# Performance work log

Measured on AMD Instinct MI355X. Metric: run time of the kernel, lower is better.

The kernel has to match this reference:

```python
import jax, jax.numpy as jnp
import numpy as np

EMBED = 1024
HEADS = 16
HEAD_DIM = EMBED // HEADS


def setup_inputs() -> dict:
    key = jax.random.key(0)
    ks = jax.random.split(key, 11)
    B, S = 2, 2048
    scale = 1.0 / np.sqrt(EMBED)
    inp = {
        'Q': jax.random.normal(ks[0], (B, S, EMBED), jnp.float32),
        'K': jax.random.normal(ks[1], (B, S, EMBED), jnp.float32),
        'V': jax.random.normal(ks[2], (B, S, EMBED), jnp.float32),
        'Wq': jax.random.normal(ks[3], (EMBED, EMBED), jnp.float32) * scale,
        'bq': jnp.zeros((EMBED,), jnp.float32),
        'Wk': jax.random.normal(ks[4], (EMBED, EMBED), jnp.float32) * scale,
        'bk': jnp.zeros((EMBED,), jnp.float32),
        'Wv': jax.random.normal(ks[5], (EMBED, EMBED), jnp.float32) * scale,
        'bv': jnp.zeros((EMBED,), jnp.float32),
        'Wo': jax.random.normal(ks[6], (EMBED, EMBED), jnp.float32) * scale,
        'bo': jnp.zeros((EMBED,), jnp.float32),
    }
    return inp


def reference(Q, K, V, Wq, bq, Wk, bk, Wv, bv, Wo, bo):
    B, Sq, _ = Q.shape
    Sk = K.shape[1]
    # linear projections (torch nn.Linear: x @ W.T + b; here W stored as [in,out])
    q = Q @ Wq + bq
    k = K @ Wk + bk
    v = V @ Wv + bv
    # [B, H, S, D]
    q = q.reshape(B, Sq, HEADS, HEAD_DIM).transpose(0, 2, 1, 3)
    k = k.reshape(B, Sk, HEADS, HEAD_DIM).transpose(0, 2, 1, 3)
    v = v.reshape(B, Sk, HEADS, HEAD_DIM).transpose(0, 2, 1, 3)
    scores = jnp.einsum('bhqd,bhkd->bhqk', q, k) / jnp.sqrt(jnp.float32(HEAD_DIM))
    attn = jax.nn.softmax(scores, axis=-1)
    out = jnp.einsum('bhqk,bhkd->bhqd', attn, v)
    out = out.transpose(0, 2, 1, 3).reshape(B, Sq, EMBED)
    return out @ Wo + bo
```

## Files before the change

### kernel.cpp

```cpp
#include <hip/hip_runtime.h>

#define EMBED 1024
#define HEADS 16
#define HDIM  64
#define BATCH 2
#define SEQ   2048
#define MTOK  (BATCH*SEQ)

typedef _Float16 half_t;
typedef __attribute__((ext_vector_type(4))) float    f32x4;
typedef __attribute__((ext_vector_type(8))) _Float16 f16x8;
typedef __attribute__((ext_vector_type(4))) _Float16 f16x4;

#define MFMA16(a,b,c) __builtin_amdgcn_mfma_f32_16x16x32_f16(a,b,c,0,0,0)

#define GLOAD_LDS16(gp, lp)                                                     \
    __builtin_amdgcn_global_load_lds(                                           \
        (const __attribute__((address_space(1))) void*)(gp),                    \
        (__attribute__((address_space(3))) void*)(lp), 16, 0, 0)

#define QSCALE 0.18033688f

__global__ __launch_bounds__(256) void wt_kernel(const float* __restrict__ W0,
                                                 const float* __restrict__ W1,
                                                 const float* __restrict__ W2,
                                                 const float* __restrict__ W3,
                                                 half_t* __restrict__ T0,
                                                 half_t* __restrict__ T1,
                                                 half_t* __restrict__ T2,
                                                 half_t* __restrict__ T3)
{
    const int z = blockIdx.z;
    const float* W = (z == 0) ? W0 : (z == 1) ? W1 : (z == 2) ? W2 : W3;
    half_t* WT     = (z == 0) ? T0 : (z == 1) ? T1 : (z == 2) ? T2 : T3;

    __shared__ float tile[64][68];
    const int t  = threadIdx.x;
    const int n0 = blockIdx.x * 64;
    const int k0 = blockIdx.y * 64;
#pragma unroll
    for (int i = 0; i < 4; ++i) {
        int f = t + 256 * i;
        int r = f >> 4, c4 = (f & 15) << 2;
        float4 v = *(const float4*)(W + (size_t)(k0 + r) * EMBED + n0 + c4);
        tile[r][c4 + 0] = v.x; tile[r][c4 + 1] = v.y;
        tile[r][c4 + 2] = v.z; tile[r][c4 + 3] = v.w;
    }
    __syncthreads();
#pragma unroll
    for (int i = 0; i < 4; ++i) {
        int f = t + 256 * i;
        int nr = f >> 4, kc = (f & 15) << 2;
        f16x4 o;
        o[0] = (half_t)tile[kc + 0][nr];
        o[1] = (half_t)tile[kc + 1][nr];
        o[2] = (half_t)tile[kc + 2][nr];
        o[3] = (half_t)tile[kc + 3][nr];
        *(f16x4*)(WT + (size_t)(n0 + nr) * EMBED + k0 + kc) = o;
    }
}

__global__ __launch_bounds__(256) void conv_kernel(const float* __restrict__ S0,
                                                   const float* __restrict__ S1,
                                                   const float* __restrict__ S2,
                                                   half_t* __restrict__ D0,
                                                   half_t* __restrict__ D1,
                                                   half_t* __restrict__ D2)
{
    const int z = blockIdx.z;
    const float* S = (z == 0) ? S0 : (z == 1) ? S1 : S2;
    half_t* D      = (z == 0) ? D0 : (z == 1) ? D1 : D2;
    size_t idx = ((size_t)blockIdx.x * 256 + threadIdx.x) * 8;
    float4 v0 = *(const float4*)(S + idx);
    float4 v1 = *(const float4*)(S + idx + 4);
    f16x8 hv;
    hv[0] = (half_t)v0.x; hv[1] = (half_t)v0.y;
    hv[2] = (half_t)v0.z; hv[3] = (half_t)v0.w;
    hv[4] = (half_t)v1.x; hv[5] = (half_t)v1.y;
    hv[6] = (half_t)v1.z; hv[7] = (half_t)v1.w;
    *(f16x8*)(D + idx) = hv;
}

__global__ __launch_bounds__(256, 3) void proj3_kernel(const half_t* __restrict__ Aq,
                                                       const half_t* __restrict__ Ak,
                                                       const half_t* __restrict__ Av,
                                                       const half_t* __restrict__ Btq,
                                                       const half_t* __restrict__ Btk,
                                                       const half_t* __restrict__ Btv,
                                                       const float*  __restrict__ bq,
                                                       const float*  __restrict__ bk,
                                                       const float*  __restrict__ bv,
                                                       half_t* __restrict__ oq,
                                                       half_t* __restrict__ ok,
                                                       half_t* __restrict__ ov)
{
    const int z = blockIdx.z;
    const half_t* A    = (z == 0) ? Aq  : (z == 1) ? Ak  : Av;
    const half_t* Bt   = (z == 0) ? Btq : (z == 1) ? Btk : Btv;
    const float*  bias = (z == 0) ? bq  : (z == 1) ? bk  : bv;
    half_t*       out  = (z == 0) ? oq  : (z == 1) ? ok  : ov;

    __shared__ half_t As[128 * 64];
    __shared__ half_t Bs[128 * 64];
    const int tid = threadIdx.x, lane = tid & 63, g = lane >> 4, ln = lane & 15;
    const int w = tid >> 6, wm = w >> 1, wn = w & 1;
    const int n0 = blockIdx.x * 128, m0 = blockIdx.y * 128;
    const int srow8 = lane >> 3, schunk = lane & 7;

    f32x4 acc[4][4];
#pragma unroll
    for (int i = 0; i < 4; ++i)
#pragma unroll
        for (int j = 0; j < 4; ++j) acc[i][j] = (f32x4){0.f, 0.f, 0.f, 0.f};

    for (int kt = 0; kt < EMBED; kt += 64) {
#pragma unroll
        for (int i = 0; i < 4; ++i) {
            int row = (i * 4 + w) * 8 + srow8;
            GLOAD_LDS16(A  + (size_t)(m0 + row) * EMBED + kt + schunk * 8,
                        (char*)As + (i * 4 + w) * 1024);
            GLOAD_LDS16(Bt + (size_t)(n0 + row) * EMBED + kt + schunk * 8,
                        (char*)Bs + (i * 4 + w) * 1024);
        }
        __syncthreads();
#pragma unroll
        for (int k2 = 0; k2 < 2; ++k2) {
            f16x8 af[4], bf[4];
#pragma unroll
            for (int mi = 0; mi < 4; ++mi)
                af[mi] = *(const f16x8*)(As + (wm * 64 + mi * 16 + ln) * 64 + k2 * 32 + g * 8);
#pragma unroll
            for (int ni = 0; ni < 4; ++ni)
                bf[ni] = *(const f16x8*)(Bs + (wn * 64 + ni * 16 + ln) * 64 + k2 * 32 + g * 8);
#pragma unroll
            for (int mi = 0; mi < 4; ++mi)
#pragma unroll
                for (int ni = 0; ni < 4; ++ni)
                    acc[mi][ni] = MFMA16(af[mi], bf[ni], acc[mi][ni]);
        }
        __syncthreads();
    }

#pragma unroll
    for (int mi = 0; mi < 4; ++mi) {
#pragma unroll
        for (int ni = 0; ni < 4; ++ni) {
            int col = n0 + wn * 64 + ni * 16 + ln;
            float bb = bias[col];
            int h = col >> 6, d = col & 63;
#pragma unroll
            for (int r = 0; r < 4; ++r) {
                int row = m0 + wm * 64 + mi * 16 + g * 4 + r;
                int b = row >> 11, s = row & 2047;
                float val = acc[mi][ni][r] + bb;
                if (z == 0) val *= QSCALE;
                if (z == 2)
                    out[((size_t)(b * HEADS + h) * HDIM + d) * SEQ + s] = (half_t)val;
                else
                    out[((size_t)(b * HEADS + h) * SEQ + s) * HDIM + d] = (half_t)val;
            }
        }
    }
}

__global__ __launch_bounds__(256, 4) void final_kernel(const half_t* __restrict__ A,
                                                       const half_t* __restrict__ Bt,
                                                       const float*  __restrict__ bias,
                                                       float* __restrict__ out)
{
    __shared__ half_t As[64 * 64];
    __shared__ half_t Bs[128 * 64];
    const int tid = threadIdx.x, lane = tid & 63, g = lane >> 4, ln = lane & 15;
    const int w = tid >> 6, wm = w >> 1, wn = w & 1;
    const int n0 = blockIdx.x * 128, m0 = blockIdx.y * 64;
    const int srow8 = lane >> 3, schunk = lane & 7;

    f32x4 acc[2][4];
#pragma unroll
    for (int i = 0; i < 2; ++i)
#pragma unroll
        for (int j = 0; j < 4; ++j) acc[i][j] = (f32x4){0.f, 0.f, 0.f, 0.f};

    for (int kt = 0; kt < EMBED; kt += 64) {
#pragma unroll
        for (int i = 0; i < 2; ++i) {
            int rg = i * 4 + w;
            GLOAD_LDS16(A + (size_t)(m0 + rg * 8 + srow8) * EMBED + kt + schunk * 8,
                        (char*)As + rg * 1024);
        }
#pragma unroll
        for (int i = 0; i < 4; ++i) {
            int rg = i * 4 + w;
            GLOAD_LDS16(Bt + (size_t)(n0 + rg * 8 + srow8) * EMBED + kt + schunk * 8,
                        (char*)Bs + rg * 1024);
        }
        __syncthreads();
#pragma unroll
        for (int k2 = 0; k2 < 2; ++k2) {
            f16x8 af[2], bf[4];
#pragma unroll
            for (int mi = 0; mi < 2; ++mi)
                af[mi] = *(const f16x8*)(As + (wm * 32 + mi * 16 + ln) * 64 + k2 * 32 + g * 8);
#pragma unroll
            for (int ni = 0; ni < 4; ++ni)
                bf[ni] = *(const f16x8*)(Bs + (wn * 64 + ni * 16 + ln) * 64 + k2 * 32 + g * 8);
#pragma unroll
            for (int mi = 0; mi < 2; ++mi)
#pragma unroll
                for (int ni = 0; ni < 4; ++ni)
                    acc[mi][ni] = MFMA16(af[mi], bf[ni], acc[mi][ni]);
        }
        __syncthreads();
    }
#pragma unroll
    for (int mi = 0; mi < 2; ++mi) {
#pragma unroll
        for (int ni = 0; ni < 4; ++ni) {
            int col = n0 + wn * 64 + ni * 16 + ln;
            float bb = bias[col];
#pragma unroll
            for (int r = 0; r < 4; ++r) {
                int row = m0 + wm * 32 + mi * 16 + g * 4 + r;
                out[(size_t)row * EMBED + col] = acc[mi][ni][r] + bb;
            }
        }
    }
}

__global__ __launch_bounds__(256, 2) void attn_kernel(const half_t* __restrict__ q,
                                                      const half_t* __restrict__ k,
                                                      const half_t* __restrict__ vt,
                                                      half_t* __restrict__ opart,
                                                      float*  __restrict__ lpart)
{
    __shared__ half_t Ks[64 * 64];
    __shared__ half_t Vs[64 * 64];
    __shared__ half_t Ps[4][32 * 72];
    const int tid = threadIdx.x, lane = tid & 63, g = lane >> 4, ln = lane & 15;
    const int w = tid >> 6;

    const int fid = blockIdx.x;
    const int j = fid & 7, t = fid >> 3;
    const int yhi = t >> 5, rem = t & 31;
    const int z = rem >> 4, x = rem & 15;
    const int bh = yhi * 8 + j;
    const int bb = bh >> 4, h = bh & 15;

    const int kv0 = z * (SEQ / 2);
    const int kvend = kv0 + SEQ / 2;
    const half_t* qh = q  + (size_t)bh * SEQ * HDIM;
    const half_t* kh = k  + (size_t)bh * SEQ * HDIM;
    const half_t* vh = vt + (size_t)bh * HDIM * SEQ;
    const int qrow0 = x * 128 + w * 32;

    f16x8 qfrag[2][2];
#pragma unroll
    for (int mt = 0; mt < 2; ++mt)
#pragma unroll
        for (int kt = 0; kt < 2; ++kt)
            qfrag[mt][kt] = *(const f16x8*)(qh + (size_t)(qrow0 + mt * 16 + ln) * HDIM + kt * 32 + g * 8);

    f32x4 accO[2][4];
#pragma unroll
    for (int mt = 0; mt < 2; ++mt)
#pragma unroll
        for (int nt = 0; nt < 4; ++nt) accO[mt][nt] = (f32x4){0.f, 0.f, 0.f, 0.f};
    float lsum[2] = {0.f, 0.f};

    const int srow0 = tid >> 3;
    const int scol16 = tid & 7;

    {
        f16x8 rK[2], rV[2];
#pragma unroll
        for (int c = 0; c < 2; ++c) {
            int row = c * 32 + srow0;
            rK[c] = *(const f16x8*)(kh + (size_t)(kv0 + row) * HDIM + scol16 * 8);
            rV[c] = *(const f16x8*)(vh + (size_t)row * SEQ + kv0 + scol16 * 8);
        }
#pragma unroll
        for (int c = 0; c < 2; ++c) {
            int row = c * 32 + srow0;
            int off = row * 128 + ((scol16 * 16) ^ ((row & 7) << 4));
            *(f16x8*)((char*)Ks + off) = rK[c];
            *(f16x8*)((char*)Vs + off) = rV[c];
        }
    }
    __syncthreads();

    for (int kv = kv0; kv < kvend; kv += 64) {
        f32x4 accT[2][4];
#pragma unroll
        for (int mt = 0; mt < 2; ++mt)
#pragma unroll
            for (int kb = 0; kb < 4; ++kb) accT[mt][kb] = (f32x4){0.f, 0.f, 0.f, 0.f};
#pragma unroll
        for (int kt = 0; kt < 2; ++kt) {
            f16x8 kf[4];
#pragma unroll
            for (int kb = 0; kb < 4; ++kb) {
                int row = kb * 16 + ln;
                kf[kb] = *(const f16x8*)((char*)Ks + row * 128 + ((kt * 64 + g * 16) ^ ((row & 7) << 4)));
            }
            __builtin_amdgcn_s_setprio(1);
#pragma unroll
            for (int mt = 0; mt < 2; ++mt)
#pragma unroll
                for (int kb = 0; kb < 4; ++kb)
                    accT[mt][kb] = MFMA16(kf[kb], qfrag[mt][kt], accT[mt][kb]);
            __builtin_amdgcn_s_setprio(0);
        }

        const bool has_next = (kv + 64) < kvend;
        f16x8 rK[2], rV[2];
        if (has_next) {
#pragma unroll
            for (int c = 0; c < 2; ++c) {
                int row = c * 32 + srow0;
                rK[c] = *(const f16x8*)(kh + (size_t)(kv + 64 + row) * HDIM + scol16 * 8);
                rV[c] = *(const f16x8*)(vh + (size_t)row * SEQ + kv + 64 + scol16 * 8);
            }
        }

#pragma unroll
        for (int mt = 0; mt < 2; ++mt) {
#pragma unroll
            for (int kb = 0; kb < 4; ++kb) {
                float p0 = __builtin_amdgcn_exp2f(accT[mt][kb][0]);
                float p1 = __builtin_amdgcn_exp2f(accT[mt][kb][1]);
                float p2 = __builtin_amdgcn_exp2f(accT[mt][kb][2]);
                float p3 = __builtin_amdgcn_exp2f(accT[mt][kb][3]);
                lsum[mt] += (p0 + p1) + (p2 + p3);
                f16x4 pv;
                pv[0] = (half_t)p0; pv[1] = (half_t)p1;
                pv[2] = (half_t)p2; pv[3] = (half_t)p3;
                *(f16x4*)(&Ps[w][(mt * 16 + ln) * 72 + kb * 16 + g * 4]) = pv;
            }
        }

#pragma unroll
        for (int kt = 0; kt < 2; ++kt) {
            f16x8 bf[4], ap[2];
#pragma unroll
            for (int nt = 0; nt < 4; ++nt) {
                int row = nt * 16 + ln;
                bf[nt] = *(const f16x8*)((char*)Vs + row * 128 + ((kt * 64 + g * 16) ^ ((row & 7) << 4)));
            }
#pragma unroll
            for (int mt = 0; mt < 2; ++mt)
                ap[mt] = *(const f16x8*)(&Ps[w][(mt * 16 + ln) * 72 + kt * 32 + g * 8]);
            __builtin_amdgcn_s_setprio(1);
#pragma unroll
            for (int mt = 0; mt < 2; ++mt)
#pragma unroll
                for (int nt = 0; nt < 4; ++nt)
                    accO[mt][nt] = MFMA16(ap[mt], bf[nt], accO[mt][nt]);
            __builtin_amdgcn_s_setprio(0);
        }

        if (has_next) {
            __syncthreads();
#pragma unroll
            for (int c = 0; c < 2; ++c) {
                int row = c * 32 + srow0;
                int off = row * 128 + ((scol16 * 16) ^ ((row & 7) << 4));
                *(f16x8*)((char*)Ks + off) = rK[c];
                *(f16x8*)((char*)Vs + off) = rV[c];
            }
            __syncthreads();
        }
    }

#pragma unroll
    for (int mt = 0; mt < 2; ++mt) {
        lsum[mt] += __shfl_xor(lsum[mt], 16);
        lsum[mt] += __shfl_xor(lsum[mt], 32);
    }

    const size_t zoff = (size_t)z * MTOK * EMBED;
#pragma unroll
    for (int mt = 0; mt < 2; ++mt) {
#pragma unroll
        for (int r = 0; r < 4; ++r) {
            int srow_o = qrow0 + mt * 16 + g * 4 + r;
#pragma unroll
            for (int nt = 0; nt < 4; ++nt) {
                int d = nt * 16 + ln;
                opart[zoff + ((size_t)(bb * SEQ + srow_o)) * EMBED + h * HDIM + d] =
                    (half_t)accO[mt][nt][r];
            }
        }
        if (g == 0)
            lpart[(size_t)z * HEADS * BATCH * SEQ + (size_t)bh * SEQ + qrow0 + mt * 16 + ln] = lsum[mt];
    }
}

__global__ __launch_bounds__(256) void combine_kernel(const half_t* __restrict__ opart,
                                                      const float*  __restrict__ lpart,
                                                      half_t* __restrict__ ao)
{
    size_t i = ((size_t)blockIdx.x * 256 + threadIdx.x) * 8;
    int token = (int)(i >> 10);
    int e = (int)(i & 1023);
    int bb = token >> 11, s = token & 2047, h = e >> 6;
    int li = (bb * HEADS + h) * SEQ + s;
    float l = lpart[li] + lpart[HEADS * BATCH * SEQ + li];
    float inv = 1.0f / l;
    f16x8 a = *(const f16x8*)(opart + i);
    f16x8 b = *(const f16x8*)(opart + (size_t)MTOK * EMBED + i);
    f16x8 o;
#pragma unroll
    for (int j = 0; j < 8; ++j)
        o[j] = (half_t)(((float)a[j] + (float)b[j]) * inv);
    *(f16x8*)(ao + i) = o;
}

extern "C" void kernel_launch(void* const* d_in, const int* in_sizes, int n_in,
                              void* d_out, int out_size, void* d_ws, size_t ws_size,
                              hipStream_t stream)
{
    const float* Q  = (const float*)d_in[0];
    const float* K  = (const float*)d_in[1];
    const float* V  = (const float*)d_in[2];
    const float* Wq = (const float*)d_in[3];
    const float* bq = (const float*)d_in[4];
    const float* Wk = (const float*)d_in[5];
    const float* bk = (const float*)d_in[6];
    const float* Wv = (const float*)d_in[7];
    const float* bv = (const float*)d_in[8];
    const float* Wo = (const float*)d_in[9];
    const float* bo = (const float*)d_in[10];
    float* out = (float*)d_out;

    half_t* ws = (half_t*)d_ws;
    const size_t WSZ = (size_t)EMBED * EMBED;
    const size_t TSZ = (size_t)MTOK * EMBED;
    half_t* WqT = ws;
    half_t* WkT = WqT + WSZ;
    half_t* WvT = WkT + WSZ;
    half_t* WoT = WvT + WSZ;
    half_t* Qc  = WoT + WSZ;
    half_t* Kc  = Qc + TSZ;
    half_t* Vc  = Kc + TSZ;
    half_t* qf  = Vc + TSZ;
    half_t* kf  = qf + TSZ;
    half_t* vT  = kf + TSZ;
    half_t* ao  = vT + TSZ;
    half_t* opart = Qc;
    float*  lpart = (float*)Vc;

    dim3 blk(256);
    wt_kernel<<<dim3(16, 16, 4), blk, 0, stream>>>(Wq, Wk, Wv, Wo, WqT, WkT, WvT, WoT);
    conv_kernel<<<dim3(2048, 1, 3), blk, 0, stream>>>(Q, K, V, Qc, Kc, Vc);

    proj3_kernel<<<dim3(EMBED / 128, MTOK / 128, 3), blk, 0, stream>>>(
        Qc, Kc, Vc, WqT, WkT, WvT, bq, bk, bv, qf, kf, vT);

    attn_kernel<<<dim3(1024), blk, 0, stream>>>(qf, kf, vT, opart, lpart);
    combine_kernel<<<dim3(2048), blk, 0, stream>>>(opart, lpart, ao);

    final_kernel<<<dim3(EMBED / 128, MTOK / 64), blk, 0, stream>>>(ao, WoT, bo, out);
}
```

Baseline: 135.6 us.

## Remove split-KV attention and fuse normalization into attention epilogue

The attention kernel now processes the full KV sequence per block instead of splitting it into two halves, normalizes by the row sum in its epilogue, and writes the final fp16 output directly. This removes the combine kernel and the round trip of partial outputs and sums through global memory. The grid halves, so fewer blocks are available for latency hiding. Separately, the transposed V store in the projection epilogue is vectorized into 4-element half stores.

```diff
diff --git a/kernel.cpp b/kernel.cpp
--- a/kernel.cpp
+++ b/kernel.cpp
@@ -148,16 +148,23 @@
             int col = n0 + wn * 64 + ni * 16 + ln;
             float bb = bias[col];
             int h = col >> 6, d = col & 63;
-#pragma unroll
-            for (int r = 0; r < 4; ++r) {
-                int row = m0 + wm * 64 + mi * 16 + g * 4 + r;
-                int b = row >> 11, s = row & 2047;
-                float val = acc[mi][ni][r] + bb;
-                if (z == 0) val *= QSCALE;
-                if (z == 2)
-                    out[((size_t)(b * HEADS + h) * HDIM + d) * SEQ + s] = (half_t)val;
-                else
+            if (z == 2) {
+                int row0 = m0 + wm * 64 + mi * 16 + g * 4;
+                int b = row0 >> 11, s = row0 & 2047;
+                f16x4 o4;
+#pragma unroll
+                for (int r = 0; r < 4; ++r)
+                    o4[r] = (half_t)(acc[mi][ni][r] + bb);
+                *(f16x4*)(out + ((size_t)(b * HEADS + h) * HDIM + d) * SEQ + s) = o4;
+            } else {
+#pragma unroll
+                for (int r = 0; r < 4; ++r) {
+                    int row = m0 + wm * 64 + mi * 16 + g * 4 + r;
+                    int b = row >> 11, s = row & 2047;
+                    float val = acc[mi][ni][r] + bb;
+                    if (z == 0) val *= QSCALE;
                     out[((size_t)(b * HEADS + h) * SEQ + s) * HDIM + d] = (half_t)val;
+                }
             }
         }
     }
@@ -230,8 +237,7 @@
 __global__ __launch_bounds__(256, 2) void attn_kernel(const half_t* __restrict__ q,
                                                       const half_t* __restrict__ k,
                                                       const half_t* __restrict__ vt,
-                                                      half_t* __restrict__ opart,
-                                                      float*  __restrict__ lpart)
+                                                      half_t* __restrict__ ao)
 {
     __shared__ half_t Ks[64 * 64];
     __shared__ half_t Vs[64 * 64];
@@ -241,13 +247,10 @@
 
     const int fid = blockIdx.x;
     const int j = fid & 7, t = fid >> 3;
-    const int yhi = t >> 5, rem = t & 31;
-    const int z = rem >> 4, x = rem & 15;
+    const int yhi = t >> 4, x = t & 15;
     const int bh = yhi * 8 + j;
     const int bb = bh >> 4, h = bh & 15;
 
-    const int kv0 = z * (SEQ / 2);
-    const int kvend = kv0 + SEQ / 2;
     const half_t* qh = q  + (size_t)bh * SEQ * HDIM;
     const half_t* kh = k  + (size_t)bh * SEQ * HDIM;
     const half_t* vh = vt + (size_t)bh * HDIM * SEQ;
@@ -275,8 +278,8 @@
 #pragma unroll
         for (int c = 0; c < 2; ++c) {
             int row = c * 32 + srow0;
-            rK[c] = *(const f16x8*)(kh + (size_t)(kv0 + row) * HDIM + scol16 * 8);
-            rV[c] = *(const f16x8*)(vh + (size_t)row * SEQ + kv0 + scol16 * 8);
+            rK[c] = *(const f16x8*)(kh + (size_t)row * HDIM + scol16 * 8);
+            rV[c] = *(const f16x8*)(vh + (size_t)row * SEQ + scol16 * 8);
         }
 #pragma unroll
         for (int c = 0; c < 2; ++c) {
@@ -288,7 +291,7 @@
     }
     __syncthreads();
 
-    for (int kv = kv0; kv < kvend; kv += 64) {
+    for (int kv = 0; kv < SEQ; kv += 64) {
         f32x4 accT[2][4];
 #pragma unroll
         for (int mt = 0; mt < 2; ++mt)
@@ -311,7 +314,7 @@
             __builtin_amdgcn_s_setprio(0);
         }
 
-        const bool has_next = (kv + 64) < kvend;
+        const bool has_next = (kv + 64) < SEQ;
         f16x8 rK[2], rV[2];
         if (has_next) {
 #pragma unroll
@@ -377,42 +380,20 @@
         lsum[mt] += __shfl_xor(lsum[mt], 32);
     }
 
-    const size_t zoff = (size_t)z * MTOK * EMBED;
 #pragma unroll
     for (int mt = 0; mt < 2; ++mt) {
 #pragma unroll
         for (int r = 0; r < 4; ++r) {
+            float linv = 1.0f / __shfl(lsum[mt], g * 4 + r);
             int srow_o = qrow0 + mt * 16 + g * 4 + r;
 #pragma unroll
             for (int nt = 0; nt < 4; ++nt) {
                 int d = nt * 16 + ln;
-                opart[zoff + ((size_t)(bb * SEQ + srow_o)) * EMBED + h * HDIM + d] =
-                    (half_t)accO[mt][nt][r];
-            }
-        }
-        if (g == 0)
-            lpart[(size_t)z * HEADS * BATCH * SEQ + (size_t)bh * SEQ + qrow0 + mt * 16 + ln] = lsum[mt];
-    }
-}
-
-__global__ __launch_bounds__(256) void combine_kernel(const half_t* __restrict__ opart,
-                                                      const float*  __restrict__ lpart,
-                                                      half_t* __restrict__ ao)
-{
-    size_t i = ((size_t)blockIdx.x * 256 + threadIdx.x) * 8;
-    int token = (int)(i >> 10);
-    int e = (int)(i & 1023);
-    int bb = token >> 11, s = token & 2047, h = e >> 6;
-    int li = (bb * HEADS + h) * SEQ + s;
-    float l = lpart[li] + lpart[HEADS * BATCH * SEQ + li];
-    float inv = 1.0f / l;
-    f16x8 a = *(const f16x8*)(opart + i);
-    f16x8 b = *(const f16x8*)(opart + (size_t)MTOK * EMBED + i);
-    f16x8 o;
-#pragma unroll
-    for (int j = 0; j < 8; ++j)
-        o[j] = (half_t)(((float)a[j] + (float)b[j]) * inv);
-    *(f16x8*)(ao + i) = o;
+                ao[((size_t)(bb * SEQ + srow_o)) * EMBED + h * HDIM + d] =
+                    (half_t)(accO[mt][nt][r] * linv);
+            }
+        }
+    }
 }
 
 extern "C" void kernel_launch(void* const* d_in, const int* in_sizes, int n_in,
@@ -446,8 +427,6 @@
     half_t* kf  = qf + TSZ;
     half_t* vT  = kf + TSZ;
     half_t* ao  = vT + TSZ;
-    half_t* opart = Qc;
-    float*  lpart = (float*)Vc;
 
     dim3 blk(256);
     wt_kernel<<<dim3(16, 16, 4), blk, 0, stream>>>(Wq, Wk, Wv, Wo, WqT, WkT, WvT, WoT);
@@ -456,8 +435,7 @@
     proj3_kernel<<<dim3(EMBED / 128, MTOK / 128, 3), blk, 0, stream>>>(
         Qc, Kc, Vc, WqT, WkT, WvT, bq, bk, bv, qf, kf, vT);
 
-    attn_kernel<<<dim3(1024), blk, 0, stream>>>(qf, kf, vT, opart, lpart);
-    combine_kernel<<<dim3(2048), blk, 0, stream>>>(opart, lpart, ao);
+    attn_kernel<<<dim3(512), blk, 0, stream>>>(qf, kf, vT, ao);
 
     final_kernel<<<dim3(EMBED / 128, MTOK / 64), blk, 0, stream>>>(ao, WoT, bo, out);
 }
```

New measurement: 125.4 us. -7.5%, faster.
